# Kernel tuning notes

Measured on AMD Instinct MI355X. Metric: run time of the kernel, lower is better.

The kernel has to match this reference:

```python
import jax, jax.numpy as jnp
import numpy as np

EPS = 1e-6

def ln2d(x, w, b):
    # LayerNorm over channel dim of NCHW, biased variance, eps=1e-6
    mu = x.mean(1, keepdims=True)
    var = ((x - mu) ** 2).mean(1, keepdims=True)
    y = (x - mu) / jnp.sqrt(var + EPS)
    return w[None, :, None, None] * y + b[None, :, None, None]

def conv1x1(x, w, b):
    # 1x1 conv == pointwise channel mix: w is [C_out, C_in]
    return jnp.einsum('nchw,oc->nohw', x, w) + b[None, :, None, None]

def setup_inputs() -> dict:
    key = jax.random.key(0)
    N, C, H, W = 4, 128, 256, 256
    ks = jax.random.split(key, 8)
    inp = {
        'msi': jax.random.normal(ks[0], (N, C, H, W), jnp.float32),
        'pan': jax.random.normal(ks[1], (N, C, H, W), jnp.float32),
        'ln_w_msi': jnp.ones((C,), jnp.float32),
        'ln_b_msi': jnp.zeros((C,), jnp.float32),
        'ln_w_pan': jnp.ones((C,), jnp.float32),
        'ln_b_pan': jnp.zeros((C,), jnp.float32),
        'w_mp1': jax.random.normal(ks[2], (C, C), jnp.float32) * 0.05,
        'b_mp1': jnp.zeros((C,), jnp.float32),
        'w_pp1': jax.random.normal(ks[3], (C, C), jnp.float32) * 0.05,
        'b_pp1': jnp.zeros((C,), jnp.float32),
        'w_mp2': jax.random.normal(ks[4], (C, C), jnp.float32) * 0.05,
        'b_mp2': jnp.zeros((C,), jnp.float32),
        'w_pp2': jax.random.normal(ks[5], (C, C), jnp.float32) * 0.05,
        'b_pp2': jnp.zeros((C,), jnp.float32),
        'beta': jax.random.normal(ks[6], (1, C, 1, 1), jnp.float32) * 0.1,
        'gamma': jax.random.normal(ks[7], (1, C, 1, 1), jnp.float32) * 0.1,
    }
    return inp

def reference(msi, pan, ln_w_msi, ln_b_msi, ln_w_pan, ln_b_pan,
              w_mp1, b_mp1, w_pp1, b_pp1, w_mp2, b_mp2, w_pp2, b_pp2,
              beta, gamma):
    C = msi.shape[1]
    scale = C ** (-0.5)
    nm = ln2d(msi, ln_w_msi, ln_b_msi)          # norm_msi(msi)
    npn = ln2d(pan, ln_w_pan, ln_b_pan)         # norm_pan(pan)
    q_msi = conv1x1(nm, w_mp1, b_mp1)           # msi_proj1(norm_msi)
    q_pan_from_msi = conv1x1(nm, w_pp1, b_pp1)  # pan_proj1(norm_msi) -- quirk in source
    q_pan = conv1x1(npn, w_pp1, b_pp1)          # pan_proj1(norm_pan)
    v_msi = conv1x1(msi, w_mp2, b_mp2)
    v_pan = conv1x1(pan, w_pp2, b_pp2)
    # per-row attention: contract channels, shared row h -> [N,H,W,W]
    attn_mp = jnp.einsum('nchw,nchv->nhwv', q_msi, q_pan) * scale
    attn_pm = jnp.einsum('nchw,nchv->nhwv', q_pan_from_msi, q_msi) * scale
    f_m2p = jnp.einsum('nhwv,nchv->nchw', jax.nn.softmax(attn_mp, axis=-1), v_pan)
    f_p2m = jnp.einsum('nhwv,nchv->nchw', jax.nn.softmax(attn_pm, axis=-1), v_msi)
    return (msi + f_m2p * beta, pan + f_p2m * gamma)
```

## Files before the change

### kernel.cpp

```cpp
#include <hip/hip_runtime.h>
#include <hip/hip_bf16.h>

typedef __attribute__((ext_vector_type(4))) float f32x4;
typedef __attribute__((ext_vector_type(8))) short s16x8;

#define NB 4
#define CHN 128
#define HH 256
#define WW 256
#define HWSZ (HH*WW)
#define TENSOR_ELEMS ((size_t)NB*CHN*HWSZ)
#define SCALE 0.08838834764831845f

__device__ __forceinline__ unsigned short f2b(float f) {
    unsigned int u = __builtin_bit_cast(unsigned int, f);
    u += 0x7fffu + ((u >> 16) & 1u);
    return (unsigned short)(u >> 16);
}
__device__ __forceinline__ unsigned int pack2(float a, float b) {
    return (unsigned int)f2b(a) | ((unsigned int)f2b(b) << 16);
}

__device__ __forceinline__ void stage_w(uint4* bufW4, const float* __restrict__ W, int t) {
    #pragma unroll
    for (int it = 0; it < 4; ++it) {
        int j = it*512 + t;
        int o = j >> 4, ch = j & 15;
        const float4* wp = (const float4*)(W + o*128 + ch*8);
        float4 a = wp[0], b = wp[1];
        uint4 u;
        u.x = pack2(a.x, a.y); u.y = pack2(a.z, a.w);
        u.z = pack2(b.x, b.y); u.w = pack2(b.z, b.w);
        bufW4[o*16 + (ch ^ (o & 7))] = u;
    }
}

__device__ __forceinline__ void gemm_tile(const uint4* bufW4, const uint4* bufB4,
                                          int wave, int lr, int lg, f32x4 acc[8]) {
    s16x8 af[4];
    int arow = wave*16 + lr;
    #pragma unroll
    for (int ks = 0; ks < 4; ++ks)
        af[ks] = __builtin_bit_cast(s16x8, bufW4[arow*16 + ((ks*4+lg) ^ (arow & 7))]);
    #pragma unroll
    for (int nt = 0; nt < 8; ++nt) {
        int brow = nt*16 + lr;
        #pragma unroll
        for (int ks = 0; ks < 4; ++ks) {
            s16x8 bf = __builtin_bit_cast(s16x8, bufB4[brow*16 + ((ks*4+lg) ^ (brow & 7))]);
            acc[nt] = __builtin_amdgcn_mfma_f32_16x16x32_bf16(af[ks], bf, acc[nt], 0, 0, 0);
        }
    }
}

__device__ __forceinline__ void epi_nchw(unsigned short* __restrict__ out, const float* __restrict__ bias,
                                         int n, int pos0, int wave, int lr, int lg, const f32x4 acc[8]) {
    int cb = wave*16 + lg*4;
    float bs[4];
    #pragma unroll
    for (int r = 0; r < 4; ++r) bs[r] = bias[cb + r];
    #pragma unroll
    for (int nt = 0; nt < 8; ++nt) {
        int p = pos0 + nt*16 + lr;
        #pragma unroll
        for (int r = 0; r < 4; ++r)
            out[((size_t)(n*CHN + cb + r))*HWSZ + p] = f2b(acc[nt][r] + bs[r]);
    }
}

__device__ __forceinline__ void epi_nhwc(unsigned short* __restrict__ out, const float* __restrict__ bias,
                                         int n, int pos0, int wave, int lr, int lg, const f32x4 acc[8]) {
    int cb = wave*16 + lg*4;
    float bs[4];
    #pragma unroll
    for (int r = 0; r < 4; ++r) bs[r] = bias[cb + r];
    #pragma unroll
    for (int nt = 0; nt < 8; ++nt) {
        size_t rowb = ((size_t)n*HWSZ + pos0 + nt*16 + lr)*CHN + cb;
        *(unsigned int*)(out + rowb)     = pack2(acc[nt][0]+bs[0], acc[nt][1]+bs[1]);
        *(unsigned int*)(out + rowb + 2) = pack2(acc[nt][2]+bs[2], acc[nt][3]+bs[3]);
    }
}

__global__ __launch_bounds__(512)
void proj_kernel(const float* __restrict__ msi, const float* __restrict__ pan,
                 const float* __restrict__ lnw_m, const float* __restrict__ lnb_m,
                 const float* __restrict__ lnw_p, const float* __restrict__ lnb_p,
                 const float* __restrict__ w_mp1, const float* __restrict__ b_mp1,
                 const float* __restrict__ w_pp1, const float* __restrict__ b_pp1,
                 const float* __restrict__ w_mp2, const float* __restrict__ b_mp2,
                 const float* __restrict__ w_pp2, const float* __restrict__ b_pp2,
                 unsigned short* __restrict__ ws_u)
{
    __shared__ uint4 bufB4[2048];
    __shared__ uint4 bufW4[2048];
    __shared__ float red[1024];
    __shared__ float s_mu[128];
    __shared__ float s_rs[128];

    const int t = threadIdx.x;
    const int isPan = blockIdx.y;
    const int gid = blockIdx.x;
    const int n = gid >> 9;
    const int pos0 = (gid & 511) << 7;

    const int pos = t & 127;
    const int cg = t >> 7;

    const float* src = isPan ? pan : msi;
    const float* lnw = isPan ? lnw_p : lnw_m;
    const float* lnb = isPan ? lnb_p : lnb_m;

    unsigned short* q_msi_t = ws_u;
    unsigned short* q_pfm_t = ws_u + TENSOR_ELEMS;
    unsigned short* q_pan_t = ws_u + 2*TENSOR_ELEMS;
    unsigned short* v_msi   = ws_u + 3*TENSOR_ELEMS;
    unsigned short* v_pan   = ws_u + 4*TENSOR_ELEMS;

    float vals[32];
    {
        const float* p = src + ((size_t)(n*CHN + cg*32))*HWSZ + pos0 + pos;
        #pragma unroll
        for (int j = 0; j < 32; ++j) vals[j] = p[(size_t)j*HWSZ];
    }
    #pragma unroll
    for (int k8 = 0; k8 < 4; ++k8) {
        uint4 u;
        u.x = pack2(vals[k8*8+0], vals[k8*8+1]);
        u.y = pack2(vals[k8*8+2], vals[k8*8+3]);
        u.z = pack2(vals[k8*8+4], vals[k8*8+5]);
        u.w = pack2(vals[k8*8+6], vals[k8*8+7]);
        int chunk = cg*4 + k8;
        bufB4[pos*16 + (chunk ^ (pos & 7))] = u;
    }
    stage_w(bufW4, isPan ? w_pp2 : w_mp2, t);
    __syncthreads();

    const int wave = t >> 6, lane = t & 63, lr = lane & 15, lg = lane >> 4;
    const f32x4 zero4 = {0.f, 0.f, 0.f, 0.f};

    f32x4 acc[8];
    #pragma unroll
    for (int i = 0; i < 8; ++i) acc[i] = zero4;
    gemm_tile(bufW4, bufB4, wave, lr, lg, acc);
    epi_nchw(isPan ? v_pan : v_msi, isPan ? b_pp2 : b_mp2, n, pos0, wave, lr, lg, acc);

    float s = 0.f, q = 0.f;
    #pragma unroll
    for (int j = 0; j < 32; ++j) { s += vals[j]; q += vals[j]*vals[j]; }
    red[t] = s; red[512 + t] = q;
    __syncthreads();
    if (t < 128) {
        float S = red[t] + red[t+128] + red[t+256] + red[t+384];
        float Q = red[512+t] + red[512+t+128] + red[512+t+256] + red[512+t+384];
        float mu = S * (1.0f/128.0f);
        float var = Q * (1.0f/128.0f) - mu*mu;
        s_mu[t] = mu;
        s_rs[t] = rsqrtf(var + 1e-6f);
    }
    __syncthreads();
    {
        float mu = s_mu[pos], rs = s_rs[pos];
        #pragma unroll
        for (int j = 0; j < 32; ++j) {
            int c = cg*32 + j;
            vals[j] = (vals[j] - mu) * rs * lnw[c] + lnb[c];
        }
    }
    #pragma unroll
    for (int k8 = 0; k8 < 4; ++k8) {
        uint4 u;
        u.x = pack2(vals[k8*8+0], vals[k8*8+1]);
        u.y = pack2(vals[k8*8+2], vals[k8*8+3]);
        u.z = pack2(vals[k8*8+4], vals[k8*8+5]);
        u.w = pack2(vals[k8*8+6], vals[k8*8+7]);
        int chunk = cg*4 + k8;
        bufB4[pos*16 + (chunk ^ (pos & 7))] = u;
    }
    stage_w(bufW4, isPan ? w_pp1 : w_mp1, t);
    __syncthreads();

    #pragma unroll
    for (int i = 0; i < 8; ++i) acc[i] = zero4;
    gemm_tile(bufW4, bufB4, wave, lr, lg, acc);
    epi_nhwc(isPan ? q_pan_t : q_msi_t, isPan ? b_pp1 : b_mp1, n, pos0, wave, lr, lg, acc);

    if (!isPan) {
        __syncthreads();
        stage_w(bufW4, w_pp1, t);
        __syncthreads();
        #pragma unroll
        for (int i = 0; i < 8; ++i) acc[i] = zero4;
        gemm_tile(bufW4, bufB4, wave, lr, lg, acc);
        epi_nhwc(q_pfm_t, b_pp1, n, pos0, wave, lr, lg, acc);
    }
}

__global__ __launch_bounds__(512)
void attn_kernel(const unsigned short* __restrict__ ws_u,
                 const float* __restrict__ msi, const float* __restrict__ pan,
                 const float* __restrict__ beta, const float* __restrict__ gamma,
                 float* __restrict__ out)
{
    __shared__ uint4 kp4[4096];
    __shared__ uint4 v4[4096];

    const int t = threadIdx.x;
    const int wave = t >> 6, lane = t & 63, lr = lane & 15, lg = lane >> 4;
    const int nh = blockIdx.x;
    const int n = nh >> 8, h = nh & 255;
    const int path = blockIdx.y;
    const int wh = blockIdx.z;

    const unsigned short* q_msi_t = ws_u;
    const unsigned short* q_pfm_t = ws_u + TENSOR_ELEMS;
    const unsigned short* q_pan_t = ws_u + 2*TENSOR_ELEMS;
    const unsigned short* v_msi   = ws_u + 3*TENSOR_ELEMS;
    const unsigned short* v_pan   = ws_u + 4*TENSOR_ELEMS;

    const unsigned short* Qp = path ? q_pfm_t : q_msi_t;
    const unsigned short* Kp = path ? q_msi_t : q_pan_t;
    const unsigned short* Vp = path ? v_msi   : v_pan;
    const float* resid = path ? pan : msi;
    const float* mul   = path ? gamma : beta;
    float* outp = out + (path ? TENSOR_ELEMS : (size_t)0);

    const size_t qkBase = (size_t)nh * (256*128);

    {
        const uint4* g = (const uint4*)(Kp + qkBase);
        #pragma unroll
        for (int it = 0; it < 8; ++it) {
            int i = it*512 + t;
            int v = i >> 4, ch = i & 15;
            kp4[v*16 + (ch ^ (v & 7))] = g[i];
        }
    }
    s16x8 qf[4];
    {
        int w = wh*128 + wave*16 + lr;
        const uint4* g = (const uint4*)(Qp + qkBase + (size_t)w*128);
        #pragma unroll
        for (int ks = 0; ks < 4; ++ks) qf[ks] = __builtin_bit_cast(s16x8, g[ks*4 + lg]);
    }
    __syncthreads();

    const f32x4 zero4 = {0.f, 0.f, 0.f, 0.f};
    f32x4 sAcc[16];
    #pragma unroll
    for (int i = 0; i < 16; ++i) sAcc[i] = zero4;
    #pragma unroll
    for (int nt = 0; nt < 16; ++nt) {
        int vrow = nt*16 + lr;
        #pragma unroll
        for (int ks = 0; ks < 4; ++ks) {
            s16x8 bf = __builtin_bit_cast(s16x8, kp4[vrow*16 + ((ks*4+lg) ^ (vrow & 7))]);
            sAcc[nt] = __builtin_amdgcn_mfma_f32_16x16x32_bf16(qf[ks], bf, sAcc[nt], 0, 0, 0);
        }
    }

    {
        const unsigned short* vb = Vp + (size_t)n*CHN*HWSZ + (size_t)h*WW;
        #pragma unroll
        for (int it = 0; it < 8; ++it) {
            int i = it*512 + t;
            int c = i >> 5, ch = i & 31;
            const uint4* g = (const uint4*)(vb + (size_t)c*HWSZ + ch*8);
            v4[c*32 + (ch ^ (c & 7))] = g[0];
        }
    }

    float mx[4] = {-1e30f, -1e30f, -1e30f, -1e30f};
    #pragma unroll
    for (int nt = 0; nt < 16; ++nt) {
        #pragma unroll
        for (int r = 0; r < 4; ++r) mx[r] = fmaxf(mx[r], sAcc[nt][r]);
    }
    #pragma unroll
    for (int m = 1; m <= 8; m <<= 1) {
        #pragma unroll
        for (int r = 0; r < 4; ++r) mx[r] = fmaxf(mx[r], __shfl_xor(mx[r], m, 64));
    }
    float sm[4] = {0.f, 0.f, 0.f, 0.f};
    #pragma unroll
    for (int nt = 0; nt < 16; ++nt) {
        #pragma unroll
        for (int r = 0; r < 4; ++r) {
            float p = __expf((sAcc[nt][r] - mx[r]) * SCALE);
            sAcc[nt][r] = p;
            sm[r] += p;
        }
    }
    #pragma unroll
    for (int m = 1; m <= 8; m <<= 1) {
        #pragma unroll
        for (int r = 0; r < 4; ++r) sm[r] += __shfl_xor(sm[r], m, 64);
    }
    float inv[4];
    #pragma unroll
    for (int r = 0; r < 4; ++r) inv[r] = 1.0f / sm[r];

    __syncthreads();

    {
        unsigned short* pbuf = (unsigned short*)kp4;
        int wl0 = wave*16 + lg*4;
        #pragma unroll
        for (int nt = 0; nt < 16; ++nt) {
            int v = nt*16 + lr;
            #pragma unroll
            for (int r = 0; r < 4; ++r) {
                int wl = wl0 + r;
                pbuf[wl*256 + (((v >> 3) ^ (wl & 7)) << 3) + (v & 7)] = f2b(sAcc[nt][r] * inv[r]);
            }
        }
    }
    __syncthreads();

    f32x4 oAcc[8];
    #pragma unroll
    for (int i = 0; i < 8; ++i) oAcc[i] = zero4;
    const int wrow = wave*16 + lr;
    #pragma unroll
    for (int ks = 0; ks < 8; ++ks) {
        s16x8 pb = __builtin_bit_cast(s16x8, kp4[wrow*32 + ((ks*4+lg) ^ (wrow & 7))]);
        #pragma unroll
        for (int mt = 0; mt < 8; ++mt) {
            int crow = mt*16 + lr;
            s16x8 av = __builtin_bit_cast(s16x8, v4[crow*32 + ((ks*4+lg) ^ (crow & 7))]);
            oAcc[mt] = __builtin_amdgcn_mfma_f32_16x16x32_bf16(av, pb, oAcc[mt], 0, 0, 0);
        }
    }

    {
        int wout = wh*128 + wave*16 + lr;
        size_t colbase = (size_t)h*WW + wout;
        #pragma unroll
        for (int mt = 0; mt < 8; ++mt) {
            int cb = mt*16 + lg*4;
            #pragma unroll
            for (int r = 0; r < 4; ++r) {
                int c = cb + r;
                size_t idx = ((size_t)(n*CHN + c))*HWSZ + colbase;
                outp[idx] = resid[idx] + oAcc[mt][r] * mul[c];
            }
        }
    }
}

extern "C" void kernel_launch(void* const* d_in, const int* in_sizes, int n_in,
                              void* d_out, int out_size, void* d_ws, size_t ws_size,
                              hipStream_t stream) {
    (void)in_sizes; (void)n_in; (void)out_size; (void)ws_size;
    const float* msi   = (const float*)d_in[0];
    const float* pan   = (const float*)d_in[1];
    const float* lnw_m = (const float*)d_in[2];
    const float* lnb_m = (const float*)d_in[3];
    const float* lnw_p = (const float*)d_in[4];
    const float* lnb_p = (const float*)d_in[5];
    const float* w_mp1 = (const float*)d_in[6];
    const float* b_mp1 = (const float*)d_in[7];
    const float* w_pp1 = (const float*)d_in[8];
    const float* b_pp1 = (const float*)d_in[9];
    const float* w_mp2 = (const float*)d_in[10];
    const float* b_mp2 = (const float*)d_in[11];
    const float* w_pp2 = (const float*)d_in[12];
    const float* b_pp2 = (const float*)d_in[13];
    const float* beta  = (const float*)d_in[14];
    const float* gamma = (const float*)d_in[15];
    unsigned short* ws_u = (unsigned short*)d_ws;
    float* out = (float*)d_out;

    proj_kernel<<<dim3(2048, 2), 512, 0, stream>>>(
        msi, pan, lnw_m, lnb_m, lnw_p, lnb_p,
        w_mp1, b_mp1, w_pp1, b_pp1, w_mp2, b_mp2, w_pp2, b_pp2, ws_u);
    attn_kernel<<<dim3(1024, 2, 2), 512, 0, stream>>>(
        ws_u, msi, pan, beta, gamma, out);
}
```

Baseline: 452.6 us.

## Halve attention LDS by splitting PV into two key halves with register-prefetched V

```diff
diff --git a/kernel.cpp b/kernel.cpp
--- a/kernel.cpp
+++ b/kernel.cpp
@@ -196,14 +196,13 @@
     }
 }
 
-__global__ __launch_bounds__(512)
+__global__ __launch_bounds__(512, 4)
 void attn_kernel(const unsigned short* __restrict__ ws_u,
                  const float* __restrict__ msi, const float* __restrict__ pan,
                  const float* __restrict__ beta, const float* __restrict__ gamma,
                  float* __restrict__ out)
 {
     __shared__ uint4 kp4[4096];
-    __shared__ uint4 v4[4096];
 
     const int t = threadIdx.x;
     const int wave = t >> 6, lane = t & 63, lr = lane & 15, lg = lane >> 4;
@@ -226,6 +225,15 @@
     float* outp = out + (path ? TENSOR_ELEMS : (size_t)0);
 
     const size_t qkBase = (size_t)nh * (256*128);
+    const unsigned short* vb = Vp + (size_t)n*CHN*HWSZ + (size_t)h*WW;
+
+    const int vc_c  = t >> 4;
+    const int vc_ch = t & 15;
+
+    uint4 vpre0[4];
+    #pragma unroll
+    for (int it = 0; it < 4; ++it)
+        vpre0[it] = *(const uint4*)(vb + (size_t)(vc_c + it*32)*HWSZ + vc_ch*8);
 
     {
         const uint4* g = (const uint4*)(Kp + qkBase);
@@ -259,17 +267,6 @@
         }
     }
 
-    {
-        const unsigned short* vb = Vp + (size_t)n*CHN*HWSZ + (size_t)h*WW;
-        #pragma unroll
-        for (int it = 0; it < 8; ++it) {
-            int i = it*512 + t;
-            int c = i >> 5, ch = i & 31;
-            const uint4* g = (const uint4*)(vb + (size_t)c*HWSZ + ch*8);
-            v4[c*32 + (ch ^ (c & 7))] = g[0];
-        }
-    }
-
     float mx[4] = {-1e30f, -1e30f, -1e30f, -1e30f};
     #pragma unroll
     for (int nt = 0; nt < 16; ++nt) {
@@ -302,32 +299,71 @@
 
     __syncthreads();
 
-    {
-        unsigned short* pbuf = (unsigned short*)kp4;
-        int wl0 = wave*16 + lg*4;
-        #pragma unroll
-        for (int nt = 0; nt < 16; ++nt) {
-            int v = nt*16 + lr;
-            #pragma unroll
-            for (int r = 0; r < 4; ++r) {
-                int wl = wl0 + r;
-                pbuf[wl*256 + (((v >> 3) ^ (wl & 7)) << 3) + (v & 7)] = f2b(sAcc[nt][r] * inv[r]);
-            }
-        }
-    }
-    __syncthreads();
+    uint4* p4h = kp4;
+    uint4* v4h = kp4 + 2048;
+    unsigned short* pbuf = (unsigned short*)p4h;
+    const int wl0 = wave*16 + lg*4;
+    const int wrow = wave*16 + lr;
 
     f32x4 oAcc[8];
     #pragma unroll
     for (int i = 0; i < 8; ++i) oAcc[i] = zero4;
-    const int wrow = wave*16 + lr;
-    #pragma unroll
-    for (int ks = 0; ks < 8; ++ks) {
-        s16x8 pb = __builtin_bit_cast(s16x8, kp4[wrow*32 + ((ks*4+lg) ^ (wrow & 7))]);
+
+    uint4 vpre1[4];
+    #pragma unroll
+    for (int it = 0; it < 4; ++it)
+        vpre1[it] = *(const uint4*)(vb + (size_t)(vc_c + it*32)*HWSZ + 128 + vc_ch*8);
+    #pragma unroll
+    for (int it = 0; it < 4; ++it) {
+        int c = vc_c + it*32;
+        v4h[c*16 + (vc_ch ^ (c & 7))] = vpre0[it];
+    }
+    #pragma unroll
+    for (int j = 0; j < 8; ++j) {
+        int v = j*16 + lr;
+        #pragma unroll
+        for (int r = 0; r < 4; ++r) {
+            int wl = wl0 + r;
+            pbuf[wl*128 + (((v >> 3) ^ (wl & 7)) << 3) + (v & 7)] = f2b(sAcc[j][r] * inv[r]);
+        }
+    }
+    __syncthreads();
+    #pragma unroll
+    for (int ks = 0; ks < 4; ++ks) {
+        int chunk = ks*4 + lg;
+        s16x8 pb = __builtin_bit_cast(s16x8, p4h[wrow*16 + (chunk ^ (wrow & 7))]);
         #pragma unroll
         for (int mt = 0; mt < 8; ++mt) {
             int crow = mt*16 + lr;
-            s16x8 av = __builtin_bit_cast(s16x8, v4[crow*32 + ((ks*4+lg) ^ (crow & 7))]);
+            s16x8 av = __builtin_bit_cast(s16x8, v4h[crow*16 + (chunk ^ (crow & 7))]);
+            oAcc[mt] = __builtin_amdgcn_mfma_f32_16x16x32_bf16(av, pb, oAcc[mt], 0, 0, 0);
+        }
+    }
+    __syncthreads();
+
+    #pragma unroll
+    for (int it = 0; it < 4; ++it) {
+        int c = vc_c + it*32;
+        v4h[c*16 + (vc_ch ^ (c & 7))] = vpre1[it];
+    }
+    #pragma unroll
+    for (int j = 0; j < 8; ++j) {
+        int v = j*16 + lr;
+        #pragma unroll
+        for (int r = 0; r < 4; ++r) {
+            int wl = wl0 + r;
+            pbuf[wl*128 + (((v >> 3) ^ (wl & 7)) << 3) + (v & 7)] = f2b(sAcc[j+8][r] * inv[r]);
+        }
+    }
+    __syncthreads();
+    #pragma unroll
+    for (int ks = 0; ks < 4; ++ks) {
+        int chunk = ks*4 + lg;
+        s16x8 pb = __builtin_bit_cast(s16x8, p4h[wrow*16 + (chunk ^ (wrow & 7))]);
+        #pragma unroll
+        for (int mt = 0; mt < 8; ++mt) {
+            int crow = mt*16 + lr;
+            s16x8 av = __builtin_bit_cast(s16x8, v4h[crow*16 + (chunk ^ (crow & 7))]);
             oAcc[mt] = __builtin_amdgcn_mfma_f32_16x16x32_bf16(av, pb, oAcc[mt], 0, 0, 0);
         }
     }
```

Result: slower. 606.2 us (+33.9%).

## Process full attention row per 1024-thread block and stream P in halves

Applied to the files above, without the earlier changes.

```diff
diff --git a/kernel.cpp b/kernel.cpp
--- a/kernel.cpp
+++ b/kernel.cpp
@@ -196,21 +196,20 @@
     }
 }
 
-__global__ __launch_bounds__(512)
+__global__ __launch_bounds__(1024, 4)
 void attn_kernel(const unsigned short* __restrict__ ws_u,
                  const float* __restrict__ msi, const float* __restrict__ pan,
                  const float* __restrict__ beta, const float* __restrict__ gamma,
                  float* __restrict__ out)
 {
-    __shared__ uint4 kp4[4096];
-    __shared__ uint4 v4[4096];
+    __shared__ uint4 regA[4096];
+    __shared__ uint4 regB[4096];
 
     const int t = threadIdx.x;
     const int wave = t >> 6, lane = t & 63, lr = lane & 15, lg = lane >> 4;
     const int nh = blockIdx.x;
     const int n = nh >> 8, h = nh & 255;
     const int path = blockIdx.y;
-    const int wh = blockIdx.z;
 
     const unsigned short* q_msi_t = ws_u;
     const unsigned short* q_pfm_t = ws_u + TENSOR_ELEMS;
@@ -226,19 +225,28 @@
     float* outp = out + (path ? TENSOR_ELEMS : (size_t)0);
 
     const size_t qkBase = (size_t)nh * (256*128);
+    const unsigned short* vb = Vp + (size_t)n*CHN*HWSZ + (size_t)h*WW;
 
     {
         const uint4* g = (const uint4*)(Kp + qkBase);
         #pragma unroll
-        for (int it = 0; it < 8; ++it) {
-            int i = it*512 + t;
+        for (int it = 0; it < 4; ++it) {
+            int i = it*1024 + t;
             int v = i >> 4, ch = i & 15;
-            kp4[v*16 + (ch ^ (v & 7))] = g[i];
+            regA[v*16 + (ch ^ (v & 7))] = g[i];
+        }
+    }
+    {
+        #pragma unroll
+        for (int it = 0; it < 4; ++it) {
+            int i = it*1024 + t;
+            int c = i >> 5, ch = i & 31;
+            regB[c*32 + (ch ^ (c & 7))] = *(const uint4*)(vb + (size_t)c*HWSZ + ch*8);
         }
     }
     s16x8 qf[4];
     {
-        int w = wh*128 + wave*16 + lr;
+        int w = wave*16 + lr;
         const uint4* g = (const uint4*)(Qp + qkBase + (size_t)w*128);
         #pragma unroll
         for (int ks = 0; ks < 4; ++ks) qf[ks] = __builtin_bit_cast(s16x8, g[ks*4 + lg]);
@@ -254,19 +262,8 @@
         int vrow = nt*16 + lr;
         #pragma unroll
         for (int ks = 0; ks < 4; ++ks) {
-            s16x8 bf = __builtin_bit_cast(s16x8, kp4[vrow*16 + ((ks*4+lg) ^ (vrow & 7))]);
+            s16x8 bf = __builtin_bit_cast(s16x8, regA[vrow*16 + ((ks*4+lg) ^ (vrow & 7))]);
             sAcc[nt] = __builtin_amdgcn_mfma_f32_16x16x32_bf16(qf[ks], bf, sAcc[nt], 0, 0, 0);
-        }
-    }
-
-    {
-        const unsigned short* vb = Vp + (size_t)n*CHN*HWSZ + (size_t)h*WW;
-        #pragma unroll
-        for (int it = 0; it < 8; ++it) {
-            int i = it*512 + t;
-            int c = i >> 5, ch = i & 31;
-            const uint4* g = (const uint4*)(vb + (size_t)c*HWSZ + ch*8);
-            v4[c*32 + (ch ^ (c & 7))] = g[0];
         }
     }
 
@@ -302,38 +299,42 @@
 
     __syncthreads();
 
-    {
-        unsigned short* pbuf = (unsigned short*)kp4;
-        int wl0 = wave*16 + lg*4;
-        #pragma unroll
-        for (int nt = 0; nt < 16; ++nt) {
-            int v = nt*16 + lr;
+    unsigned short* pbuf = (unsigned short*)regA;
+    const int wl0 = wave*16 + lg*4;
+    const int wrow = wave*16 + lr;
+
+    f32x4 oAcc[8];
+    #pragma unroll
+    for (int i = 0; i < 8; ++i) oAcc[i] = zero4;
+
+    #pragma unroll
+    for (int vh = 0; vh < 2; ++vh) {
+        #pragma unroll
+        for (int j = 0; j < 8; ++j) {
+            int v = j*16 + lr;
             #pragma unroll
             for (int r = 0; r < 4; ++r) {
                 int wl = wl0 + r;
-                pbuf[wl*256 + (((v >> 3) ^ (wl & 7)) << 3) + (v & 7)] = f2b(sAcc[nt][r] * inv[r]);
+                pbuf[wl*128 + (((v >> 3) ^ (wl & 7)) << 3) + (v & 7)] = f2b(sAcc[vh*8 + j][r] * inv[r]);
             }
         }
-    }
-    __syncthreads();
-
-    f32x4 oAcc[8];
-    #pragma unroll
-    for (int i = 0; i < 8; ++i) oAcc[i] = zero4;
-    const int wrow = wave*16 + lr;
-    #pragma unroll
-    for (int ks = 0; ks < 8; ++ks) {
-        s16x8 pb = __builtin_bit_cast(s16x8, kp4[wrow*32 + ((ks*4+lg) ^ (wrow & 7))]);
-        #pragma unroll
-        for (int mt = 0; mt < 8; ++mt) {
-            int crow = mt*16 + lr;
-            s16x8 av = __builtin_bit_cast(s16x8, v4[crow*32 + ((ks*4+lg) ^ (crow & 7))]);
-            oAcc[mt] = __builtin_amdgcn_mfma_f32_16x16x32_bf16(av, pb, oAcc[mt], 0, 0, 0);
-        }
-    }
-
-    {
-        int wout = wh*128 + wave*16 + lr;
+        __syncthreads();
+        #pragma unroll
+        for (int ks = 0; ks < 4; ++ks) {
+            int chunk = ks*4 + lg;
+            s16x8 pb = __builtin_bit_cast(s16x8, regA[wrow*16 + (chunk ^ (wrow & 7))]);
+            #pragma unroll
+            for (int mt = 0; mt < 8; ++mt) {
+                int crow = mt*16 + lr;
+                s16x8 av = __builtin_bit_cast(s16x8, regB[crow*32 + ((vh*16 + chunk) ^ (crow & 7))]);
+                oAcc[mt] = __builtin_amdgcn_mfma_f32_16x16x32_bf16(av, pb, oAcc[mt], 0, 0, 0);
+            }
+        }
+        if (vh == 0) __syncthreads();
+    }
+
+    {
+        int wout = wave*16 + lr;
         size_t colbase = (size_t)h*WW + wout;
         #pragma unroll
         for (int mt = 0; mt < 8; ++mt) {
@@ -374,6 +375,6 @@
     proj_kernel<<<dim3(2048, 2), 512, 0, stream>>>(
         msi, pan, lnw_m, lnb_m, lnw_p, lnb_p,
         w_mp1, b_mp1, w_pp1, b_pp1, w_mp2, b_mp2, w_pp2, b_pp2, ws_u);
-    attn_kernel<<<dim3(1024, 2, 2), 512, 0, stream>>>(
+    attn_kernel<<<dim3(1024, 2), 1024, 0, stream>>>(
         ws_u, msi, pan, beta, gamma, out);
 }
```

Result: slower. 525.5 us (+16.1%).

## Coalesce NCHW epilogue stores via LDS staging and prefetch residual tiles

Applied to the files above, without the earlier changes.

```diff
diff --git a/kernel.cpp b/kernel.cpp
--- a/kernel.cpp
+++ b/kernel.cpp
@@ -19,6 +19,9 @@
 }
 __device__ __forceinline__ unsigned int pack2(float a, float b) {
     return (unsigned int)f2b(a) | ((unsigned int)f2b(b) << 16);
+}
+__device__ __forceinline__ float b2f(unsigned int lo16) {
+    return __builtin_bit_cast(float, lo16 << 16);
 }
 
 __device__ __forceinline__ void stage_w(uint4* bufW4, const float* __restrict__ W, int t) {
@@ -53,21 +56,6 @@
     }
 }
 
-__device__ __forceinline__ void epi_nchw(unsigned short* __restrict__ out, const float* __restrict__ bias,
-                                         int n, int pos0, int wave, int lr, int lg, const f32x4 acc[8]) {
-    int cb = wave*16 + lg*4;
-    float bs[4];
-    #pragma unroll
-    for (int r = 0; r < 4; ++r) bs[r] = bias[cb + r];
-    #pragma unroll
-    for (int nt = 0; nt < 8; ++nt) {
-        int p = pos0 + nt*16 + lr;
-        #pragma unroll
-        for (int r = 0; r < 4; ++r)
-            out[((size_t)(n*CHN + cb + r))*HWSZ + p] = f2b(acc[nt][r] + bs[r]);
-    }
-}
-
 __device__ __forceinline__ void epi_nhwc(unsigned short* __restrict__ out, const float* __restrict__ bias,
                                          int n, int pos0, int wave, int lr, int lg, const f32x4 acc[8]) {
     int cb = wave*16 + lg*4;
@@ -77,8 +65,10 @@
     #pragma unroll
     for (int nt = 0; nt < 8; ++nt) {
         size_t rowb = ((size_t)n*HWSZ + pos0 + nt*16 + lr)*CHN + cb;
-        *(unsigned int*)(out + rowb)     = pack2(acc[nt][0]+bs[0], acc[nt][1]+bs[1]);
-        *(unsigned int*)(out + rowb + 2) = pack2(acc[nt][2]+bs[2], acc[nt][3]+bs[3]);
+        uint2 u;
+        u.x = pack2(acc[nt][0]+bs[0], acc[nt][1]+bs[1]);
+        u.y = pack2(acc[nt][2]+bs[2], acc[nt][3]+bs[3]);
+        *(uint2*)(out + rowb) = u;
     }
 }
 
@@ -92,11 +82,14 @@
                  const float* __restrict__ w_pp2, const float* __restrict__ b_pp2,
                  unsigned short* __restrict__ ws_u)
 {
-    __shared__ uint4 bufB4[2048];
-    __shared__ uint4 bufW4[2048];
+    __shared__ uint4 pool[4096];
     __shared__ float red[1024];
     __shared__ float s_mu[128];
     __shared__ float s_rs[128];
+
+    uint4* bufB4 = pool;
+    uint4* bufW4 = pool + 2048;
+    unsigned short* vbounce = (unsigned short*)pool;
 
     const int t = threadIdx.x;
     const int isPan = blockIdx.y;
@@ -143,13 +136,13 @@
     #pragma unroll
     for (int i = 0; i < 8; ++i) acc[i] = zero4;
     gemm_tile(bufW4, bufB4, wave, lr, lg, acc);
-    epi_nchw(isPan ? v_pan : v_msi, isPan ? b_pp2 : b_mp2, n, pos0, wave, lr, lg, acc);
 
     float s = 0.f, q = 0.f;
     #pragma unroll
     for (int j = 0; j < 32; ++j) { s += vals[j]; q += vals[j]*vals[j]; }
     red[t] = s; red[512 + t] = q;
     __syncthreads();
+
     if (t < 128) {
         float S = red[t] + red[t+128] + red[t+256] + red[t+384];
         float Q = red[512+t] + red[512+t+128] + red[512+t+256] + red[512+t+384];
@@ -158,7 +151,32 @@
         s_mu[t] = mu;
         s_rs[t] = rsqrtf(var + 1e-6f);
     }
-    __syncthreads();
+    {
+        const float* bias = isPan ? b_pp2 : b_mp2;
+        int cb = wave*16 + lg*4;
+        float bs[4];
+        #pragma unroll
+        for (int r = 0; r < 4; ++r) bs[r] = bias[cb + r];
+        #pragma unroll
+        for (int nt = 0; nt < 8; ++nt) {
+            int p = nt*16 + lr;
+            #pragma unroll
+            for (int r = 0; r < 4; ++r)
+                vbounce[(cb + r)*136 + p] = f2b(acc[nt][r] + bs[r]);
+        }
+    }
+    __syncthreads();
+
+    {
+        unsigned short* vout = isPan ? v_pan : v_msi;
+        #pragma unroll
+        for (int i = 0; i < 4; ++i) {
+            int fl = i*512 + t;
+            int c = fl >> 4, k = fl & 15;
+            uint4 u = *(const uint4*)(vbounce + c*136 + k*8);
+            *(uint4*)(vout + ((size_t)(n*CHN + c))*HWSZ + pos0 + k*8) = u;
+        }
+    }
     {
         float mu = s_mu[pos], rs = s_rs[pos];
         #pragma unroll
@@ -167,6 +185,8 @@
             vals[j] = (vals[j] - mu) * rs * lnw[c] + lnb[c];
         }
     }
+    __syncthreads();
+
     #pragma unroll
     for (int k8 = 0; k8 < 4; ++k8) {
         uint4 u;
@@ -196,7 +216,7 @@
     }
 }
 
-__global__ __launch_bounds__(512)
+__global__ __launch_bounds__(512, 2)
 void attn_kernel(const unsigned short* __restrict__ ws_u,
                  const float* __restrict__ msi, const float* __restrict__ pan,
                  const float* __restrict__ beta, const float* __restrict__ gamma,
@@ -207,10 +227,12 @@
 
     const int t = threadIdx.x;
     const int wave = t >> 6, lane = t & 63, lr = lane & 15, lg = lane >> 4;
-    const int nh = blockIdx.x;
+    const int bid = blockIdx.x;
+    const int sib = (bid >> 3) & 3;
+    const int nh = (bid >> 5) * 8 + (bid & 7);
+    const int path = sib >> 1;
+    const int wh = sib & 1;
     const int n = nh >> 8, h = nh & 255;
-    const int path = blockIdx.y;
-    const int wh = blockIdx.z;
 
     const unsigned short* q_msi_t = ws_u;
     const unsigned short* q_pfm_t = ws_u + TENSOR_ELEMS;
@@ -226,6 +248,7 @@
     float* outp = out + (path ? TENSOR_ELEMS : (size_t)0);
 
     const size_t qkBase = (size_t)nh * (256*128);
+    const unsigned short* vb = Vp + (size_t)n*CHN*HWSZ + (size_t)h*WW;
 
     {
         const uint4* g = (const uint4*)(Kp + qkBase);
@@ -260,13 +283,25 @@
     }
 
     {
-        const unsigned short* vb = Vp + (size_t)n*CHN*HWSZ + (size_t)h*WW;
         #pragma unroll
         for (int it = 0; it < 8; ++it) {
             int i = it*512 + t;
             int c = i >> 5, ch = i & 31;
             const uint4* g = (const uint4*)(vb + (size_t)c*HWSZ + ch*8);
             v4[c*32 + (ch ^ (c & 7))] = g[0];
+        }
+    }
+
+    f32x4 rsdA[4], rsdB[4];
+    {
+        const float* rb = resid + (size_t)n*CHN*HWSZ + (size_t)h*WW + wh*128;
+        #pragma unroll
+        for (int i = 0; i < 4; ++i) {
+            int fl = i*512 + t;
+            int c = fl >> 4, k = fl & 15;
+            const float* p = rb + (size_t)c*HWSZ + k*8;
+            rsdA[i] = *(const f32x4*)p;
+            rsdB[i] = *(const f32x4*)(p + 4);
         }
     }
 
@@ -331,19 +366,42 @@
             oAcc[mt] = __builtin_amdgcn_mfma_f32_16x16x32_bf16(av, pb, oAcc[mt], 0, 0, 0);
         }
     }
-
-    {
-        int wout = wh*128 + wave*16 + lr;
-        size_t colbase = (size_t)h*WW + wout;
+    __syncthreads();
+
+    {
+        unsigned short* obuf = (unsigned short*)kp4;
+        int wloc = wave*16 + lr;
         #pragma unroll
         for (int mt = 0; mt < 8; ++mt) {
             int cb = mt*16 + lg*4;
             #pragma unroll
-            for (int r = 0; r < 4; ++r) {
-                int c = cb + r;
-                size_t idx = ((size_t)(n*CHN + c))*HWSZ + colbase;
-                outp[idx] = resid[idx] + oAcc[mt][r] * mul[c];
-            }
+            for (int r = 0; r < 4; ++r)
+                obuf[(cb + r)*136 + wloc] = f2b(oAcc[mt][r]);
+        }
+    }
+    __syncthreads();
+
+    {
+        const unsigned short* obuf = (const unsigned short*)kp4;
+        float* ob = outp + (size_t)n*CHN*HWSZ + (size_t)h*WW + wh*128;
+        #pragma unroll
+        for (int i = 0; i < 4; ++i) {
+            int fl = i*512 + t;
+            int c = fl >> 4, k = fl & 15;
+            uint4 u = *(const uint4*)(obuf + c*136 + k*8);
+            float mc = mul[c];
+            f32x4 o0, o1;
+            o0[0] = rsdA[i][0] + b2f(u.x & 0xffffu) * mc;
+            o0[1] = rsdA[i][1] + b2f(u.x >> 16) * mc;
+            o0[2] = rsdA[i][2] + b2f(u.y & 0xffffu) * mc;
+            o0[3] = rsdA[i][3] + b2f(u.y >> 16) * mc;
+            o1[0] = rsdB[i][0] + b2f(u.z & 0xffffu) * mc;
+            o1[1] = rsdB[i][1] + b2f(u.z >> 16) * mc;
+            o1[2] = rsdB[i][2] + b2f(u.w & 0xffffu) * mc;
+            o1[3] = rsdB[i][3] + b2f(u.w >> 16) * mc;
+            float* p = ob + (size_t)c*HWSZ + k*8;
+            *(f32x4*)p = o0;
+            *(f32x4*)(p + 4) = o1;
         }
     }
 }
@@ -374,6 +432,6 @@
     proj_kernel<<<dim3(2048, 2), 512, 0, stream>>>(
         msi, pan, lnw_m, lnb_m, lnw_p, lnb_p,
         w_mp1, b_mp1, w_pp1, b_pp1, w_mp2, b_mp2, w_pp2, b_pp2, ws_u);
-    attn_kernel<<<dim3(1024, 2, 2), 512, 0, stream>>>(
+    attn_kernel<<<dim3(4096), 512, 0, stream>>>(
         ws_u, msi, pan, beta, gamma, out);
 }
```

Result: faster. 403.6 us (-10.8%).
